# Kernel tuning notes

Measured on AMD Instinct MI355X. Metric: run time of the kernel, lower is better.

Reference implementation:

```python
import jax, jax.numpy as jnp
import numpy as np

V_SIZE = 32000
D = 1024
H = 16
HS = D // H          # 64
L = 4
T_BLOCK = 2048
B, T = 1, 2048
FF = 4 * D           # 4096
R_H = int(HS * 0.25)   # 16, per-head SVF rank
R_P = int(D * 0.25)    # 256, proj SVF rank
R_F = int(min(D, FF) * 0.25)  # 256, ffn SVF rank
STD = 0.02
EPS = 1e-5


def _ln(x, w, b):
    m = jnp.mean(x, axis=-1, keepdims=True)
    v = jnp.mean(jnp.square(x - m), axis=-1, keepdims=True)
    return (x - m) * jax.lax.rsqrt(v + EPS) * w + b


def _svf(x, Vw, z, Uw):
    # Vw: [r, in], z: [r], Uw: [out, r]  ->  ((x @ V^T) * z) @ U^T
    return ((x @ Vw.T) * z) @ Uw.T


def setup_inputs() -> dict:
    key = jax.random.key(0)
    ks = jax.random.split(key, 16)
    n = lambda k, shape: (jax.random.normal(k, shape, dtype=jnp.float32) * STD)
    inp = {
        "idx": jax.random.randint(ks[0], (B, T), 0, V_SIZE),
        "tok_emb": n(ks[1], (V_SIZE, D)),
        "pos_emb": n(ks[2], (T_BLOCK, D)),
        "ln1_w": jnp.ones((L, D)), "ln1_b": jnp.zeros((L, D)),
        "ln2_w": jnp.ones((L, D)), "ln2_b": jnp.zeros((L, D)),
        # kqv SVF factors stacked: axis0=layer, axis1=(k,q,v), axis2=head
        "kqv_V": n(ks[3], (L, 3, H, R_H, D)),
        "kqv_z": jnp.ones((L, 3, H, R_H)),
        "kqv_U": n(ks[4], (L, 3, H, HS, R_H)),
        "proj_V": n(ks[5], (L, R_P, D)),
        "proj_z": jnp.ones((L, R_P)),
        "proj_U": n(ks[6], (L, D, R_P)),
        "f1_V": n(ks[7], (L, R_F, D)),
        "f1_z": jnp.ones((L, R_F)),
        "f1_U": n(ks[8], (L, FF, R_F)),
        "f2_V": n(ks[9], (L, R_F, FF)),
        "f2_z": jnp.ones((L, R_F)),
        "f2_U": n(ks[10], (L, D, R_F)),
        "lnf_w": jnp.ones((D,)), "lnf_b": jnp.zeros((D,)),
        "lm_w": n(ks[11], (V_SIZE, D)),
    }
    return inp


def reference(idx, tok_emb, pos_emb, ln1_w, ln1_b, ln2_w, ln2_b,
              kqv_V, kqv_z, kqv_U, proj_V, proj_z, proj_U,
              f1_V, f1_z, f1_U, f2_V, f2_z, f2_U, lnf_w, lnf_b, lm_w):
    Bq, Tq = idx.shape
    x = tok_emb[idx] + pos_emb[:Tq]  # [B,T,D]
    causal = jnp.tril(jnp.ones((Tq, Tq), dtype=bool))
    for l in range(L):
        h = _ln(x, ln1_w[l], ln1_b[l])
        # per-head SVF: V projection, z scale, U projection (k,q,v in one einsum)
        t = jnp.einsum('btd,ghrd->gbthr', h, kqv_V[l]) * kqv_z[l][:, None, None]
        kqv = jnp.einsum('gbthr,ghsr->gbhts', t, kqv_U[l])  # [3,B,H,T,HS]
        k, q, v = kqv[0], kqv[1], kqv[2]
        wei = jnp.einsum('bhts,bhus->bhtu', q, k) * (HS ** -0.5)
        wei = jnp.where(causal, wei, -jnp.inf)
        wei = jax.nn.softmax(wei, axis=-1)
        att = jnp.einsum('bhtu,bhus->bhts', wei, v)           # [B,H,T,HS]
        att = att.transpose(0, 2, 1, 3).reshape(Bq, Tq, D)     # concat heads
        x = x + _svf(att, proj_V[l], proj_z[l], proj_U[l])
        h2 = _ln(x, ln2_w[l], ln2_b[l])
        ff = _svf(h2, f1_V[l], f1_z[l], f1_U[l])
        ff = jax.nn.gelu(ff, approximate=False)
        x = x + _svf(ff, f2_V[l], f2_z[l], f2_U[l])
    x = _ln(x, lnf_w, lnf_b)
    logits = x @ lm_w.T  # [B,T,vocab]
    return logits
```

## Files before the change

### kernel.cpp

```cpp
#include <hip/hip_runtime.h>
#include <hip/hip_bf16.h>


#define T_SEQ 2048
#define DMODEL 1024
#define NHEAD 16
#define HSZ 64
#define NLAYER 4
#define FFDIM 4096
#define RH 16
#define RP 256
#define RF 256
#define VOCAB 32000
#define NKQV (3 * NHEAD * RH)

typedef short short8 __attribute__((ext_vector_type(8)));
typedef float f32x4 __attribute__((ext_vector_type(4)));
typedef unsigned int uint_t;
typedef unsigned short ushort_t;

__device__ __forceinline__ float bfbits2f(uint_t bits16_in_low) {
    uint_t b = bits16_in_low << 16;
    float f;
    __builtin_memcpy(&f, &b, 4);
    return f;
}
__device__ __forceinline__ ushort_t f2bfu(float f) {
    union { __hip_bfloat16 b; ushort_t u; } cv;
    cv.b = __float2bfloat16(f);
    return cv.u;
}
__device__ __forceinline__ uint_t pack2bf(float a, float b) {
    return (uint_t)f2bfu(a) | ((uint_t)f2bfu(b) << 16);
}

__device__ __forceinline__ void gld16(const __hip_bfloat16* g, short* l) {
    __builtin_amdgcn_global_load_lds(
        (const __attribute__((address_space(1))) void*)g,
        (__attribute__((address_space(3))) void*)l, 16, 0, 0);
}

__global__ __launch_bounds__(256) void cvt_k(const float* __restrict__ in,
                                             __hip_bfloat16* __restrict__ out, int n4) {
    int i = blockIdx.x * 256 + threadIdx.x;
    if (i >= n4) return;
    float4 v = ((const float4*)in)[i];
    ushort4 o;
    o.x = f2bfu(v.x); o.y = f2bfu(v.y); o.z = f2bfu(v.z); o.w = f2bfu(v.w);
    ((ushort4*)out)[i] = o;
}

__global__ __launch_bounds__(256) void embed_k(const int* __restrict__ idx,
                                               const float* __restrict__ tok,
                                               const float* __restrict__ pos,
                                               float* __restrict__ x) {
    int i = blockIdx.x * 256 + threadIdx.x;
    int d4 = i & (DMODEL / 4 - 1);
    int t = i >> 8;
    int tk = idx[t];
    float4 a = ((const float4*)(tok + (size_t)tk * DMODEL))[d4];
    float4 p = ((const float4*)(pos + (size_t)t * DMODEL))[d4];
    a.x += p.x; a.y += p.y; a.z += p.z; a.w += p.w;
    ((float4*)(x + (size_t)t * DMODEL))[d4] = a;
}

__global__ __launch_bounds__(256) void ln_k(const float* __restrict__ xin,
                                            const float* __restrict__ w,
                                            const float* __restrict__ b,
                                            __hip_bfloat16* __restrict__ out) {
    const int row = blockIdx.x, tid = threadIdx.x;
    const float4 v = ((const float4*)(xin + (size_t)row * DMODEL))[tid];
    float s = v.x + v.y + v.z + v.w;
    float q = v.x * v.x + v.y * v.y + v.z * v.z + v.w * v.w;
    for (int off = 32; off; off >>= 1) { s += __shfl_xor(s, off); q += __shfl_xor(q, off); }
    __shared__ float rs_[4], rq_[4];
    if ((tid & 63) == 0) { rs_[tid >> 6] = s; rq_[tid >> 6] = q; }
    __syncthreads();
    s = rs_[0] + rs_[1] + rs_[2] + rs_[3];
    q = rq_[0] + rq_[1] + rq_[2] + rq_[3];
    const float mean = s * (1.f / DMODEL);
    const float var = q * (1.f / DMODEL) - mean * mean;
    const float rstd = rsqrtf(var + 1e-5f);
    const float4 wv = ((const float4*)w)[tid];
    const float4 bv = ((const float4*)b)[tid];
    ushort4 o;
    o.x = f2bfu((v.x - mean) * rstd * wv.x + bv.x);
    o.y = f2bfu((v.y - mean) * rstd * wv.y + bv.y);
    o.z = f2bfu((v.z - mean) * rstd * wv.z + bv.z);
    o.w = f2bfu((v.w - mean) * rstd * wv.w + bv.w);
    ((ushort4*)out)[(size_t)row * (DMODEL / 4) + tid] = o;
}

template <int BM, int BN, int MODE>
__global__ __launch_bounds__(256) void gemm_t(const __hip_bfloat16* __restrict__ A,
                                              const __hip_bfloat16* __restrict__ B,
                                              const float* __restrict__ colscale,
                                              __hip_bfloat16* __restrict__ Cb,
                                              float* __restrict__ Cf,
                                              int M, int N, int K) {
    constexpr int WM = (BN >= 128) ? 2 : 4;
    constexpr int WN = 4 / WM;
    constexpr int TM = BM / WM / 16;
    constexpr int TN = BN / WN / 16;
    constexpr int IA = BM / 32;
    constexpr int IB = BN / 32;
    __shared__ short As[BM * 64];
    __shared__ short Bs[BN * 64];
    const int tid = threadIdx.x;
    const int w = tid >> 6, ln = tid & 63, lr = ln & 15, lg = ln >> 4;
    const int GM = M / BM;

    const int nwg = gridDim.x;
    const int cpx = nwg >> 3;
    const int wg = (blockIdx.x & 7) * cpx + (blockIdx.x >> 3);
    const int bm = wg % GM, bn = wg / GM;
    const int wm = w / WN, wn = w % WN;

    f32x4 acc[TM][TN] = {};

    const int srow = tid >> 3;
    const int scol = (((tid & 7) ^ ((tid >> 3) & 7)) * 8);
    const __hip_bfloat16* Ag = A + (size_t)(bm * BM + srow) * K + scol;
    const __hip_bfloat16* Bg = B + (size_t)(bn * BN + srow) * K + scol;

    for (int kt = 0; kt < K; kt += 64) {
        __syncthreads();
#pragma unroll
        for (int i = 0; i < IA; ++i)
            gld16(Ag + (size_t)(i * 32) * K + kt, &As[i * 2048 + w * 512]);
#pragma unroll
        for (int i = 0; i < IB; ++i)
            gld16(Bg + (size_t)(i * 32) * K + kt, &Bs[i * 2048 + w * 512]);
        __syncthreads();

#pragma unroll
        for (int kk = 0; kk < 2; ++kk) {
            short8 af[TM], bf[TN];
#pragma unroll
            for (int m = 0; m < TM; ++m) {
                const int row = wm * (BM / WM) + m * 16 + lr;
                af[m] = *(const short8*)&As[row * 64 + (((kk * 4 + lg) ^ (lr & 7)) * 8)];
            }
#pragma unroll
            for (int n = 0; n < TN; ++n) {
                const int row = wn * (BN / WN) + n * 16 + lr;
                bf[n] = *(const short8*)&Bs[row * 64 + (((kk * 4 + lg) ^ (lr & 7)) * 8)];
            }
#pragma unroll
            for (int m = 0; m < TM; ++m)
#pragma unroll
                for (int n = 0; n < TN; ++n)
                    acc[m][n] = __builtin_amdgcn_mfma_f32_16x16x32_bf16(af[m], bf[n], acc[m][n], 0, 0, 0);
        }
    }

#pragma unroll
    for (int n = 0; n < TN; ++n) {
        const int col = bn * BN + wn * (BN / WN) + n * 16 + lr;
        float cs = 1.0f;
        if (MODE == 0 && colscale) cs = colscale[col];
#pragma unroll
        for (int m = 0; m < TM; ++m) {
#pragma unroll
            for (int rr = 0; rr < 4; ++rr) {
                const int row = bm * BM + wm * (BM / WM) + m * 16 + lg * 4 + rr;
                float v = acc[m][n][rr];
                const size_t o = (size_t)row * N + col;
                if (MODE == 0) {
                    Cb[o] = __float2bfloat16(v * cs);
                } else if (MODE == 1) {
                    v = 0.5f * v * (1.0f + erff(v * 0.70710678118654752f));
                    Cb[o] = __float2bfloat16(v);
                } else if (MODE == 2) {
                    Cf[o] += v;
                } else {
                    Cf[o] = v;
                }
            }
        }
    }
}

__global__ __launch_bounds__(256) void kqv2_k(const __hip_bfloat16* __restrict__ t1,
                                              const __hip_bfloat16* __restrict__ U,
                                              __hip_bfloat16* __restrict__ kqv) {
    size_t i = (size_t)blockIdx.x * 256 + threadIdx.x;
    int s = (int)(i & 63);
    size_t rest = i >> 6;
    int t = (int)(rest & (T_SEQ - 1));
    int gh = (int)(rest >> 11);
    const short8* trow = (const short8*)(t1 + (size_t)t * NKQV + gh * RH);
    const short8* urow = (const short8*)(U + ((size_t)gh * HSZ + s) * RH);
    short8 ta = trow[0], tb = trow[1];
    short8 ua = urow[0], ub = urow[1];
    float acc = 0.f;
#pragma unroll
    for (int j = 0; j < 8; ++j) {
        acc += bfbits2f((ushort_t)ta[j]) * bfbits2f((ushort_t)ua[j]);
        acc += bfbits2f((ushort_t)tb[j]) * bfbits2f((ushort_t)ub[j]);
    }
    kqv[i] = __float2bfloat16(acc);
}

__global__ __launch_bounds__(256) void ktile_k(const __hip_bfloat16* __restrict__ kb,
                                               __hip_bfloat16* __restrict__ kb2) {
    const int it = blockIdx.x, h = blockIdx.y, tid = threadIdx.x;
    const int wv = tid >> 6, ln = tid & 63;
    const int lr = ln & 15, lg = ln >> 4;
#pragma unroll
    for (int q2 = 0; q2 < 2; ++q2) {
        const int c = wv * 2 + q2, g = c >> 1, half = c & 1;
        short8 v = *(const short8*)(kb + ((size_t)h * T_SEQ + it * 64 + g * 16 + lr) * HSZ + half * 32 + lg * 8);
        *(short8*)(kb2 + (((size_t)h * 32 + it) * 8 + c) * 512 + (size_t)ln * 8) = v;
    }
}

__global__ __launch_bounds__(256) void vtrans_k(const __hip_bfloat16* __restrict__ vb,
                                                __hip_bfloat16* __restrict__ vt2) {
    __shared__ short Ts[64][72];
    const int ti = blockIdx.x, h = blockIdx.y, tid = threadIdx.x;
    const int tl = tid >> 2, sc = (tid & 3) * 16;
    const short* src = (const short*)(vb + ((size_t)h * T_SEQ + ti * 64 + tl) * HSZ + sc);
    short8 a = ((const short8*)src)[0];
    short8 b = ((const short8*)src)[1];
#pragma unroll
    for (int j = 0; j < 8; ++j) { Ts[sc + j][tl] = a[j]; Ts[sc + 8 + j][tl] = b[j]; }
    __syncthreads();
    const int c = tid >> 5, r5 = tid & 31;
    const int dt = c >> 1, half = c & 1;
#pragma unroll
    for (int k2 = 0; k2 < 2; ++k2) {
        const int ln2 = r5 * 2 + k2;
        const int d = dt * 16 + (ln2 & 15);
        const int ub = half * 32 + ((ln2 >> 4) * 8);
        short8 o;
#pragma unroll
        for (int j = 0; j < 8; ++j) o[j] = Ts[d][ub + j];
        *(short8*)(vt2 + (((size_t)h * 32 + ti) * 8 + c) * 512 + (size_t)ln2 * 8) = o;
    }
}

__global__ __launch_bounds__(256) void attn_k(const __hip_bfloat16* __restrict__ qb,
                                              const __hip_bfloat16* __restrict__ kb2,
                                              const __hip_bfloat16* __restrict__ vt2,
                                              __hip_bfloat16* __restrict__ attout) {
    __shared__ short P_s[2][4][16 * 72];
    const int tid = threadIdx.x, w = tid >> 6, ln = tid & 63;
    const int lr = ln & 15, lg = ln >> 4;
    const int f = blockIdx.y * 32 + blockIdx.x;
    const int h = ((f & 7) << 1) | ((f >> 3) & 1);
    const int bi = f >> 4;
    const int t0 = bi * 16 + w * 512;
    const size_t hb = (size_t)h * T_SEQ;
    const size_t hB = (size_t)h * 32;

    short8 qf0 = *(const short8*)(qb + (hb + t0 + lr) * HSZ + lg * 8);
    short8 qf1 = *(const short8*)(qb + (hb + t0 + lr) * HSZ + 32 + lg * 8);

    f32x4 acc[4] = {};
    float mrun = -3e38f, lrun = 0.f;
    int pbuf = 0;

    short8 kf[4][2];
#pragma unroll
    for (int g = 0; g < 4; ++g) {
        kf[g][0] = *(const short8*)(kb2 + (hB * 8 + g * 2 + 0) * 512 + (size_t)ln * 8);
        kf[g][1] = *(const short8*)(kb2 + (hB * 8 + g * 2 + 1) * 512 + (size_t)ln * 8);
    }

    for (int u0 = 0; u0 <= t0 + 15; u0 += 64) {
        const int it = u0 >> 6;
        f32x4 st[4];
#pragma unroll
        for (int g = 0; g < 4; ++g) {
            f32x4 z = {};
            z = __builtin_amdgcn_mfma_f32_16x16x32_bf16(kf[g][0], qf0, z, 0, 0, 0);
            st[g] = __builtin_amdgcn_mfma_f32_16x16x32_bf16(kf[g][1], qf1, z, 0, 0, 0);
        }

        const int un = u0 + 64;
        if (un <= t0 + 15) {
            const int itn = it + 1;
#pragma unroll
            for (int g = 0; g < 4; ++g) {
                kf[g][0] = *(const short8*)(kb2 + ((hB + itn) * 8 + g * 2 + 0) * 512 + (size_t)ln * 8);
                kf[g][1] = *(const short8*)(kb2 + ((hB + itn) * 8 + g * 2 + 1) * 512 + (size_t)ln * 8);
            }
        }
        short8 vf[4][2];
#pragma unroll
        for (int dt = 0; dt < 4; ++dt) {
            vf[dt][0] = *(const short8*)(vt2 + ((hB + it) * 8 + dt * 2 + 0) * 512 + (size_t)ln * 8);
            vf[dt][1] = *(const short8*)(vt2 + ((hB + it) * 8 + dt * 2 + 1) * 512 + (size_t)ln * 8);
        }

        const int qg = t0 + lr;
        float sv[16];
#pragma unroll
        for (int g = 0; g < 4; ++g) {
            const bool needm = (u0 + g * 16 + 15 > t0);
#pragma unroll
            for (int r = 0; r < 4; ++r) {
                float v = st[g][r] * 0.125f;
                if (needm && (u0 + g * 16 + lg * 4 + r > qg)) v = -1e30f;
                sv[g * 4 + r] = v;
            }
        }
        float tm = sv[0];
#pragma unroll
        for (int j = 1; j < 16; ++j) tm = fmaxf(tm, sv[j]);
        tm = fmaxf(tm, __shfl_xor(tm, 16));
        tm = fmaxf(tm, __shfl_xor(tm, 32));
        const float mnew = fmaxf(mrun, tm);
        const float corr = __expf(mrun - mnew);
        float pv[16];
        float ls = 0.f;
#pragma unroll
        for (int j = 0; j < 16; ++j) { pv[j] = __expf(sv[j] - mnew); ls += pv[j]; }
        ls += __shfl_xor(ls, 16);
        ls += __shfl_xor(ls, 32);
        lrun = lrun * corr + ls;
#pragma unroll
        for (int dt = 0; dt < 4; ++dt) acc[dt] *= corr;

        uint_t* pw = (uint_t*)P_s[pbuf][w];
        const int wb = lr * 36 + lg * 2;
#pragma unroll
        for (int g = 0; g < 4; ++g) {
            pw[wb + g * 8 + 0] = pack2bf(pv[g * 4 + 0], pv[g * 4 + 1]);
            pw[wb + g * 8 + 1] = pack2bf(pv[g * 4 + 2], pv[g * 4 + 3]);
        }
        asm volatile("s_waitcnt lgkmcnt(0)" ::: "memory");
        short8 pf0 = *(const short8*)(&P_s[pbuf][w][lr * 72 + lg * 8]);
        short8 pf1 = *(const short8*)(&P_s[pbuf][w][lr * 72 + 32 + lg * 8]);

#pragma unroll
        for (int dt = 0; dt < 4; ++dt) {
            acc[dt] = __builtin_amdgcn_mfma_f32_16x16x32_bf16(vf[dt][0], pf0, acc[dt], 0, 0, 0);
            acc[dt] = __builtin_amdgcn_mfma_f32_16x16x32_bf16(vf[dt][1], pf1, acc[dt], 0, 0, 0);
        }

        mrun = mnew;
        pbuf ^= 1;
    }

    const float inv = 1.f / lrun;
#pragma unroll
    for (int dt = 0; dt < 4; ++dt) {
#pragma unroll
        for (int r = 0; r < 4; r += 2) {
            uint_t pk = pack2bf(acc[dt][r] * inv, acc[dt][r + 1] * inv);
            *(uint_t*)(attout + (size_t)(t0 + lr) * DMODEL + h * HSZ + dt * 16 + lg * 4 + r) = pk;
        }
    }
}

extern "C" void kernel_launch(void* const* d_in, const int* in_sizes, int n_in,
                              void* d_out, int out_size, void* d_ws, size_t ws_size,
                              hipStream_t stream) {
    const int* idx = (const int*)d_in[0];
    const float* tok_emb = (const float*)d_in[1];
    const float* pos_emb = (const float*)d_in[2];
    const float* ln1_w = (const float*)d_in[3];
    const float* ln1_b = (const float*)d_in[4];
    const float* ln2_w = (const float*)d_in[5];
    const float* ln2_b = (const float*)d_in[6];
    const float* kqv_V = (const float*)d_in[7];
    const float* kqv_z = (const float*)d_in[8];
    const float* kqv_U = (const float*)d_in[9];
    const float* proj_V = (const float*)d_in[10];
    const float* proj_z = (const float*)d_in[11];
    const float* proj_U = (const float*)d_in[12];
    const float* f1_V = (const float*)d_in[13];
    const float* f1_z = (const float*)d_in[14];
    const float* f1_U = (const float*)d_in[15];
    const float* f2_V = (const float*)d_in[16];
    const float* f2_z = (const float*)d_in[17];
    const float* f2_U = (const float*)d_in[18];
    const float* lnf_w = (const float*)d_in[19];
    const float* lnf_b = (const float*)d_in[20];
    const float* lm_w = (const float*)d_in[21];

    char* W = (char*)d_ws;
    float* x = (float*)W;                 W += (size_t)T_SEQ * DMODEL * 4;
    __hip_bfloat16* hbuf = (__hip_bfloat16*)W; W += (size_t)T_SEQ * DMODEL * 2;
    __hip_bfloat16* t1 = (__hip_bfloat16*)W;   W += (size_t)T_SEQ * NKQV * 2;
    __hip_bfloat16* kqvb = (__hip_bfloat16*)W; W += (size_t)3 * NHEAD * T_SEQ * HSZ * 2;
    __hip_bfloat16* kb2 = (__hip_bfloat16*)W;  W += (size_t)NHEAD * T_SEQ * HSZ * 2;
    __hip_bfloat16* vt2 = (__hip_bfloat16*)W;  W += (size_t)NHEAD * HSZ * T_SEQ * 2;
    __hip_bfloat16* attb = (__hip_bfloat16*)W; W += (size_t)T_SEQ * DMODEL * 2;
    __hip_bfloat16* ffb = (__hip_bfloat16*)W;  W += (size_t)T_SEQ * FFDIM * 2;
    __hip_bfloat16* wkV = (__hip_bfloat16*)W;  W += (size_t)NLAYER * NKQV * DMODEL * 2;
    __hip_bfloat16* wkU = (__hip_bfloat16*)W;  W += (size_t)NLAYER * 3 * NHEAD * HSZ * RH * 2;
    __hip_bfloat16* wpV = (__hip_bfloat16*)W;  W += (size_t)NLAYER * RP * DMODEL * 2;
    __hip_bfloat16* wpU = (__hip_bfloat16*)W;  W += (size_t)NLAYER * DMODEL * RP * 2;
    __hip_bfloat16* w1V = (__hip_bfloat16*)W;  W += (size_t)NLAYER * RF * DMODEL * 2;
    __hip_bfloat16* w1U = (__hip_bfloat16*)W;  W += (size_t)NLAYER * FFDIM * RF * 2;
    __hip_bfloat16* w2V = (__hip_bfloat16*)W;  W += (size_t)NLAYER * RF * FFDIM * 2;
    __hip_bfloat16* w2U = (__hip_bfloat16*)W;  W += (size_t)NLAYER * DMODEL * RF * 2;
    __hip_bfloat16* wlm = (__hip_bfloat16*)W;  W += (size_t)VOCAB * DMODEL * 2;

    auto cvt = [&](const float* src, __hip_bfloat16* dst, size_t n) {
        int n4 = (int)(n / 4);
        cvt_k<<<dim3((n4 + 255) / 256), dim3(256), 0, stream>>>(src, dst, n4);
    };
    cvt(kqv_V, wkV, (size_t)NLAYER * NKQV * DMODEL);
    cvt(kqv_U, wkU, (size_t)NLAYER * 3 * NHEAD * HSZ * RH);
    cvt(proj_V, wpV, (size_t)NLAYER * RP * DMODEL);
    cvt(proj_U, wpU, (size_t)NLAYER * DMODEL * RP);
    cvt(f1_V, w1V, (size_t)NLAYER * RF * DMODEL);
    cvt(f1_U, w1U, (size_t)NLAYER * FFDIM * RF);
    cvt(f2_V, w2V, (size_t)NLAYER * RF * FFDIM);
    cvt(f2_U, w2U, (size_t)NLAYER * DMODEL * RF);
    cvt(lm_w, wlm, (size_t)VOCAB * DMODEL);

    embed_k<<<dim3(T_SEQ * DMODEL / 4 / 256), dim3(256), 0, stream>>>(idx, tok_emb, pos_emb, x);

    const int M = T_SEQ;
    for (int l = 0; l < NLAYER; ++l) {
        ln_k<<<dim3(T_SEQ), dim3(256), 0, stream>>>(x, ln1_w + l * DMODEL, ln1_b + l * DMODEL, hbuf);
        gemm_t<64, 64, 0><<<dim3((M / 64) * (NKQV / 64)), dim3(256), 0, stream>>>(
            hbuf, wkV + (size_t)l * NKQV * DMODEL, kqv_z + (size_t)l * NKQV,
            t1, nullptr, M, NKQV, DMODEL);
        kqv2_k<<<dim3(3 * NHEAD * T_SEQ * HSZ / 256), dim3(256), 0, stream>>>(
            t1, wkU + (size_t)l * 3 * NHEAD * HSZ * RH, kqvb);
        {
            const __hip_bfloat16* kk = kqvb;
            const __hip_bfloat16* qq = kqvb + (size_t)NHEAD * T_SEQ * HSZ;
            const __hip_bfloat16* vv = kqvb + (size_t)2 * NHEAD * T_SEQ * HSZ;
            ktile_k<<<dim3(T_SEQ / 64, NHEAD), dim3(256), 0, stream>>>(kk, kb2);
            vtrans_k<<<dim3(T_SEQ / 64, NHEAD), dim3(256), 0, stream>>>(vv, vt2);
            attn_k<<<dim3(T_SEQ / 64, NHEAD), dim3(256), 0, stream>>>(qq, kb2, vt2, attb);
        }
        gemm_t<64, 64, 0><<<dim3((M / 64) * (RP / 64)), dim3(256), 0, stream>>>(
            attb, wpV + (size_t)l * RP * DMODEL, proj_z + (size_t)l * RP,
            t1, nullptr, M, RP, DMODEL);
        gemm_t<128, 128, 2><<<dim3((M / 128) * (DMODEL / 128)), dim3(256), 0, stream>>>(
            t1, wpU + (size_t)l * DMODEL * RP, nullptr,
            nullptr, x, M, DMODEL, RP);
        ln_k<<<dim3(T_SEQ), dim3(256), 0, stream>>>(x, ln2_w + l * DMODEL, ln2_b + l * DMODEL, hbuf);
        gemm_t<64, 64, 0><<<dim3((M / 64) * (RF / 64)), dim3(256), 0, stream>>>(
            hbuf, w1V + (size_t)l * RF * DMODEL, f1_z + (size_t)l * RF,
            t1, nullptr, M, RF, DMODEL);
        gemm_t<128, 128, 1><<<dim3((M / 128) * (FFDIM / 128)), dim3(256), 0, stream>>>(
            t1, w1U + (size_t)l * FFDIM * RF, nullptr,
            ffb, nullptr, M, FFDIM, RF);
        gemm_t<64, 64, 0><<<dim3((M / 64) * (RF / 64)), dim3(256), 0, stream>>>(
            ffb, w2V + (size_t)l * RF * FFDIM, f2_z + (size_t)l * RF,
            t1, nullptr, M, RF, FFDIM);
        gemm_t<128, 128, 2><<<dim3((M / 128) * (DMODEL / 128)), dim3(256), 0, stream>>>(
            t1, w2U + (size_t)l * DMODEL * RF, nullptr,
            nullptr, x, M, DMODEL, RF);
    }
    ln_k<<<dim3(T_SEQ), dim3(256), 0, stream>>>(x, lnf_w, lnf_b, hbuf);
    gemm_t<128, 128, 3><<<dim3((M / 128) * (VOCAB / 128)), dim3(256), 0, stream>>>(
        hbuf, wlm, nullptr, nullptr, (float*)d_out, M, VOCAB, DMODEL);
}
```

Before: 1.199 ms.

## Fuse K/V retiling into kqv2 epilogue, batch weight casts, use exp2 softmax

The kqv2 kernel now writes Q, K and V straight into the tiled and transposed layouts the attention kernel reads. This removes the separate ktile and vtrans kernels and the intermediate kqv buffer round trip. The nine weight-conversion launches are merged into one kernel that walks a table of segments. The softmax folds log2(e) into the score scale and uses exp2f. The cost is scattered 2-byte stores in kqv2 and a per-thread segment search in the conversion kernel.

```diff
diff --git a/kernel.cpp b/kernel.cpp
--- a/kernel.cpp
+++ b/kernel.cpp
@@ -40,14 +40,25 @@
         (__attribute__((address_space(3))) void*)l, 16, 0, 0);
 }
 
-__global__ __launch_bounds__(256) void cvt_k(const float* __restrict__ in,
-                                             __hip_bfloat16* __restrict__ out, int n4) {
+struct CvtArgs {
+    const float* s[9];
+    __hip_bfloat16* d[9];
+    int n4[9];
+};
+__global__ __launch_bounds__(256) void cvtall_k(CvtArgs a, int total4) {
     int i = blockIdx.x * 256 + threadIdx.x;
-    if (i >= n4) return;
-    float4 v = ((const float4*)in)[i];
-    ushort4 o;
-    o.x = f2bfu(v.x); o.y = f2bfu(v.y); o.z = f2bfu(v.z); o.w = f2bfu(v.w);
-    ((ushort4*)out)[i] = o;
+    if (i >= total4) return;
+#pragma unroll
+    for (int k = 0; k < 9; ++k) {
+        if (i < a.n4[k]) {
+            float4 v = ((const float4*)a.s[k])[i];
+            ushort4 o;
+            o.x = f2bfu(v.x); o.y = f2bfu(v.y); o.z = f2bfu(v.z); o.w = f2bfu(v.w);
+            ((ushort4*)a.d[k])[i] = o;
+            return;
+        }
+        i -= a.n4[k];
+    }
 }
 
 __global__ __launch_bounds__(256) void embed_k(const int* __restrict__ idx,
@@ -183,7 +194,9 @@
 
 __global__ __launch_bounds__(256) void kqv2_k(const __hip_bfloat16* __restrict__ t1,
                                               const __hip_bfloat16* __restrict__ U,
-                                              __hip_bfloat16* __restrict__ kqv) {
+                                              __hip_bfloat16* __restrict__ qb,
+                                              __hip_bfloat16* __restrict__ kb2,
+                                              __hip_bfloat16* __restrict__ vt2) {
     size_t i = (size_t)blockIdx.x * 256 + threadIdx.x;
     int s = (int)(i & 63);
     size_t rest = i >> 6;
@@ -199,44 +212,20 @@
         acc += bfbits2f((ushort_t)ta[j]) * bfbits2f((ushort_t)ua[j]);
         acc += bfbits2f((ushort_t)tb[j]) * bfbits2f((ushort_t)ub[j]);
     }
-    kqv[i] = __float2bfloat16(acc);
-}
-
-__global__ __launch_bounds__(256) void ktile_k(const __hip_bfloat16* __restrict__ kb,
-                                               __hip_bfloat16* __restrict__ kb2) {
-    const int it = blockIdx.x, h = blockIdx.y, tid = threadIdx.x;
-    const int wv = tid >> 6, ln = tid & 63;
-    const int lr = ln & 15, lg = ln >> 4;
-#pragma unroll
-    for (int q2 = 0; q2 < 2; ++q2) {
-        const int c = wv * 2 + q2, g = c >> 1, half = c & 1;
-        short8 v = *(const short8*)(kb + ((size_t)h * T_SEQ + it * 64 + g * 16 + lr) * HSZ + half * 32 + lg * 8);
-        *(short8*)(kb2 + (((size_t)h * 32 + it) * 8 + c) * 512 + (size_t)ln * 8) = v;
-    }
-}
-
-__global__ __launch_bounds__(256) void vtrans_k(const __hip_bfloat16* __restrict__ vb,
-                                                __hip_bfloat16* __restrict__ vt2) {
-    __shared__ short Ts[64][72];
-    const int ti = blockIdx.x, h = blockIdx.y, tid = threadIdx.x;
-    const int tl = tid >> 2, sc = (tid & 3) * 16;
-    const short* src = (const short*)(vb + ((size_t)h * T_SEQ + ti * 64 + tl) * HSZ + sc);
-    short8 a = ((const short8*)src)[0];
-    short8 b = ((const short8*)src)[1];
-#pragma unroll
-    for (int j = 0; j < 8; ++j) { Ts[sc + j][tl] = a[j]; Ts[sc + 8 + j][tl] = b[j]; }
-    __syncthreads();
-    const int c = tid >> 5, r5 = tid & 31;
-    const int dt = c >> 1, half = c & 1;
-#pragma unroll
-    for (int k2 = 0; k2 < 2; ++k2) {
-        const int ln2 = r5 * 2 + k2;
-        const int d = dt * 16 + (ln2 & 15);
-        const int ub = half * 32 + ((ln2 >> 4) * 8);
-        short8 o;
-#pragma unroll
-        for (int j = 0; j < 8; ++j) o[j] = Ts[d][ub + j];
-        *(short8*)(vt2 + (((size_t)h * 32 + ti) * 8 + c) * 512 + (size_t)ln2 * 8) = o;
+    const ushort_t val = f2bfu(acc);
+    const int g = gh >> 4, h = gh & 15;
+    if (g == 1) {
+        ((ushort_t*)qb)[((size_t)h * T_SEQ + t) * HSZ + s] = val;
+    } else if (g == 0) {
+        const int tile = t >> 6, gg = (t >> 4) & 3, lr = t & 15;
+        const int half = s >> 5, lg = (s >> 3) & 3, j = s & 7;
+        const int c = gg * 2 + half, ln = lg * 16 + lr;
+        ((ushort_t*)kb2)[(((size_t)h * 32 + tile) * 8 + c) * 512 + ln * 8 + j] = val;
+    } else {
+        const int tile = t >> 6, half = (t >> 5) & 1, lg2 = (t >> 3) & 3, j2 = t & 7;
+        const int dt = s >> 4, lr2 = s & 15;
+        const int c = dt * 2 + half, ln = lg2 * 16 + lr2;
+        ((ushort_t*)vt2)[(((size_t)h * 32 + tile) * 8 + c) * 512 + ln * 8 + j2] = val;
     }
 }
 
@@ -253,6 +242,7 @@
     const int t0 = bi * 16 + w * 512;
     const size_t hb = (size_t)h * T_SEQ;
     const size_t hB = (size_t)h * 32;
+    const float SCL = 0.18033688011112042f;
 
     short8 qf0 = *(const short8*)(qb + (hb + t0 + lr) * HSZ + lg * 8);
     short8 qf1 = *(const short8*)(qb + (hb + t0 + lr) * HSZ + 32 + lg * 8);
@@ -301,7 +291,7 @@
             const bool needm = (u0 + g * 16 + 15 > t0);
 #pragma unroll
             for (int r = 0; r < 4; ++r) {
-                float v = st[g][r] * 0.125f;
+                float v = st[g][r] * SCL;
                 if (needm && (u0 + g * 16 + lg * 4 + r > qg)) v = -1e30f;
                 sv[g * 4 + r] = v;
             }
@@ -312,11 +302,11 @@
         tm = fmaxf(tm, __shfl_xor(tm, 16));
         tm = fmaxf(tm, __shfl_xor(tm, 32));
         const float mnew = fmaxf(mrun, tm);
-        const float corr = __expf(mrun - mnew);
+        const float corr = exp2f(mrun - mnew);
         float pv[16];
         float ls = 0.f;
 #pragma unroll
-        for (int j = 0; j < 16; ++j) { pv[j] = __expf(sv[j] - mnew); ls += pv[j]; }
+        for (int j = 0; j < 16; ++j) { pv[j] = exp2f(sv[j] - mnew); ls += pv[j]; }
         ls += __shfl_xor(ls, 16);
         ls += __shfl_xor(ls, 32);
         lrun = lrun * corr + ls;
@@ -385,7 +375,7 @@
     float* x = (float*)W;                 W += (size_t)T_SEQ * DMODEL * 4;
     __hip_bfloat16* hbuf = (__hip_bfloat16*)W; W += (size_t)T_SEQ * DMODEL * 2;
     __hip_bfloat16* t1 = (__hip_bfloat16*)W;   W += (size_t)T_SEQ * NKQV * 2;
-    __hip_bfloat16* kqvb = (__hip_bfloat16*)W; W += (size_t)3 * NHEAD * T_SEQ * HSZ * 2;
+    __hip_bfloat16* qbuf = (__hip_bfloat16*)W; W += (size_t)NHEAD * T_SEQ * HSZ * 2;
     __hip_bfloat16* kb2 = (__hip_bfloat16*)W;  W += (size_t)NHEAD * T_SEQ * HSZ * 2;
     __hip_bfloat16* vt2 = (__hip_bfloat16*)W;  W += (size_t)NHEAD * HSZ * T_SEQ * 2;
     __hip_bfloat16* attb = (__hip_bfloat16*)W; W += (size_t)T_SEQ * DMODEL * 2;
@@ -400,19 +390,21 @@
     __hip_bfloat16* w2U = (__hip_bfloat16*)W;  W += (size_t)NLAYER * DMODEL * RF * 2;
     __hip_bfloat16* wlm = (__hip_bfloat16*)W;  W += (size_t)VOCAB * DMODEL * 2;
 
-    auto cvt = [&](const float* src, __hip_bfloat16* dst, size_t n) {
-        int n4 = (int)(n / 4);
-        cvt_k<<<dim3((n4 + 255) / 256), dim3(256), 0, stream>>>(src, dst, n4);
-    };
-    cvt(kqv_V, wkV, (size_t)NLAYER * NKQV * DMODEL);
-    cvt(kqv_U, wkU, (size_t)NLAYER * 3 * NHEAD * HSZ * RH);
-    cvt(proj_V, wpV, (size_t)NLAYER * RP * DMODEL);
-    cvt(proj_U, wpU, (size_t)NLAYER * DMODEL * RP);
-    cvt(f1_V, w1V, (size_t)NLAYER * RF * DMODEL);
-    cvt(f1_U, w1U, (size_t)NLAYER * FFDIM * RF);
-    cvt(f2_V, w2V, (size_t)NLAYER * RF * FFDIM);
-    cvt(f2_U, w2U, (size_t)NLAYER * DMODEL * RF);
-    cvt(lm_w, wlm, (size_t)VOCAB * DMODEL);
+    {
+        CvtArgs a;
+        a.s[0] = kqv_V;  a.d[0] = wkV;  a.n4[0] = (int)((size_t)NLAYER * NKQV * DMODEL / 4);
+        a.s[1] = kqv_U;  a.d[1] = wkU;  a.n4[1] = (int)((size_t)NLAYER * 3 * NHEAD * HSZ * RH / 4);
+        a.s[2] = proj_V; a.d[2] = wpV;  a.n4[2] = (int)((size_t)NLAYER * RP * DMODEL / 4);
+        a.s[3] = proj_U; a.d[3] = wpU;  a.n4[3] = (int)((size_t)NLAYER * DMODEL * RP / 4);
+        a.s[4] = f1_V;   a.d[4] = w1V;  a.n4[4] = (int)((size_t)NLAYER * RF * DMODEL / 4);
+        a.s[5] = f1_U;   a.d[5] = w1U;  a.n4[5] = (int)((size_t)NLAYER * FFDIM * RF / 4);
+        a.s[6] = f2_V;   a.d[6] = w2V;  a.n4[6] = (int)((size_t)NLAYER * RF * FFDIM / 4);
+        a.s[7] = f2_U;   a.d[7] = w2U;  a.n4[7] = (int)((size_t)NLAYER * DMODEL * RF / 4);
+        a.s[8] = lm_w;   a.d[8] = wlm;  a.n4[8] = (int)((size_t)VOCAB * DMODEL / 4);
+        int total4 = 0;
+        for (int k = 0; k < 9; ++k) total4 += a.n4[k];
+        cvtall_k<<<dim3((total4 + 255) / 256), dim3(256), 0, stream>>>(a, total4);
+    }
 
     embed_k<<<dim3(T_SEQ * DMODEL / 4 / 256), dim3(256), 0, stream>>>(idx, tok_emb, pos_emb, x);
 
@@ -423,15 +415,8 @@
             hbuf, wkV + (size_t)l * NKQV * DMODEL, kqv_z + (size_t)l * NKQV,
             t1, nullptr, M, NKQV, DMODEL);
         kqv2_k<<<dim3(3 * NHEAD * T_SEQ * HSZ / 256), dim3(256), 0, stream>>>(
-            t1, wkU + (size_t)l * 3 * NHEAD * HSZ * RH, kqvb);
-        {
-            const __hip_bfloat16* kk = kqvb;
-            const __hip_bfloat16* qq = kqvb + (size_t)NHEAD * T_SEQ * HSZ;
-            const __hip_bfloat16* vv = kqvb + (size_t)2 * NHEAD * T_SEQ * HSZ;
-            ktile_k<<<dim3(T_SEQ / 64, NHEAD), dim3(256), 0, stream>>>(kk, kb2);
-            vtrans_k<<<dim3(T_SEQ / 64, NHEAD), dim3(256), 0, stream>>>(vv, vt2);
-            attn_k<<<dim3(T_SEQ / 64, NHEAD), dim3(256), 0, stream>>>(qq, kb2, vt2, attb);
-        }
+            t1, wkU + (size_t)l * 3 * NHEAD * HSZ * RH, qbuf, kb2, vt2);
+        attn_k<<<dim3(T_SEQ / 64, NHEAD), dim3(256), 0, stream>>>(qbuf, kb2, vt2, attb);
         gemm_t<64, 64, 0><<<dim3((M / 64) * (RP / 64)), dim3(256), 0, stream>>>(
             attb, wpV + (size_t)l * RP * DMODEL, proj_z + (size_t)l * RP,
             t1, nullptr, M, RP, DMODEL);
```

Result: no change. 1.177 ms (-1.8%).
